# Kernel tuning notes

Measured on AMD Instinct MI355X. Metric: run time of the kernel, lower is better.

## Reference

```python
import jax, jax.numpy as jnp
import numpy as np

B, HI, WI, DIM = 4, 128, 128, 128
HO, WO = HI // 2, WI // 2
NUM_ITERS = 3
EPS_LN, EPS_A = 1e-5, 1e-6


def _nbr_idx(H, W):
    # NATTEN kernel_size=3 neighborhood with border clamping: window center is
    # clip(i, 1, H-2) so every position sees exactly 9 neighbors.
    r = 1
    ci = jnp.clip(jnp.arange(H), r, H - 1 - r)
    cj = jnp.clip(jnp.arange(W), r, W - 1 - r)
    off = jnp.arange(-1, 2)
    ri = ci[:, None] + off[None, :]  # (H,3)
    rj = cj[:, None] + off[None, :]  # (W,3)
    nbr = jnp.broadcast_to(ri[:, None, :, None], (H, W, 3, 3)).reshape(H, W, 9)
    nbc = jnp.broadcast_to(rj[None, :, None, :], (H, W, 3, 3)).reshape(H, W, 9)
    return nbr, nbc


def _ln(x, g, b):
    mu = jnp.mean(x, -1, keepdims=True)
    var = jnp.mean(jnp.square(x - mu), -1, keepdims=True)
    return (x - mu) * jax.lax.rsqrt(var + EPS_LN) * g + b


def setup_inputs() -> dict:
    key = jax.random.key(0)
    ks = jax.random.split(key, 10)
    s = DIM ** -0.5
    return {
        "x": jax.random.normal(ks[0], (B, HI * WI, DIM), jnp.float32),
        "conv_w": jax.random.normal(ks[1], (DIM, DIM, 3, 3), jnp.float32) * (2.0 / (DIM * 9)) ** 0.5,
        "q_w": jax.random.normal(ks[2], (DIM, DIM), jnp.float32) * s,
        "k_w": jax.random.normal(ks[3], (DIM, DIM), jnp.float32) * s,
        "v_w": jax.random.normal(ks[4], (DIM, DIM), jnp.float32) * s,
        "mlp_w1": jax.random.normal(ks[5], (DIM, 2 * DIM), jnp.float32) * s,
        "mlp_b1": jnp.zeros((2 * DIM,), jnp.float32),
        "mlp_w2": jax.random.normal(ks[6], (2 * DIM, DIM), jnp.float32) * (2 * DIM) ** -0.5,
        "mlp_b2": jnp.zeros((DIM,), jnp.float32),
        "ln_in_g": jnp.ones((DIM,), jnp.float32),
        "ln_in_b": jnp.zeros((DIM,), jnp.float32),
        "ln_out_g": jnp.ones((DIM,), jnp.float32),
        "ln_out_b": jnp.zeros((DIM,), jnp.float32),
        "tau": jnp.asarray(np.log(DIM ** -0.5), jnp.float32),
        "rpb": jax.random.normal(ks[7], (4, 9), jnp.float32) * 0.02,
    }


def reference(x, conv_w, q_w, k_w, v_w, mlp_w1, mlp_b1, mlp_w2, mlp_b2,
              ln_in_g, ln_in_b, ln_out_g, ln_out_b, tau, rpb):
    Bx = x.shape[0]
    nbr, nbc = _nbr_idx(HO, WO)
    q_idx = (nbr * WO + nbc).reshape(HO * WO, 9)  # flat seed index of each neighbor

    def to_groups(t):  # (B, Hi*Wi, D) -> (B, 4, Ho, Wo, D); 4 = 2x2 patch pixels (row-major)
        m = t.transpose(0, 2, 1).reshape(Bx, DIM, HO, 2, WO, 2)
        return m.transpose(0, 3, 5, 2, 4, 1).reshape(Bx, 4, HO, WO, DIM)

    k = to_groups(_ln(x, ln_in_g, ln_in_b) @ k_w)
    v = to_groups(x @ v_w)
    v_nb = v[:, :, nbr, nbc, :]  # (B,4,Ho,Wo,9,D) value neighborhoods (loop-invariant)

    x_map = x.transpose(0, 2, 1).reshape(Bx, DIM, HI, WI)
    seed = jax.lax.conv_general_dilated(x_map, conv_w, (2, 2), ((1, 1), (1, 1)),
                                        dimension_numbers=('NCHW', 'OIHW', 'NCHW'))
    x_out = _ln(seed.reshape(Bx, DIM, HO * WO).transpose(0, 2, 1), ln_out_g, ln_out_b)

    scale = jnp.exp(tau)
    flat_idx = jnp.broadcast_to(q_idx[None], (4, HO * WO, 9)).reshape(-1)
    attn = A_col = None
    for _ in range(NUM_ITERS):
        q = _ln(x_out, ln_out_g, ln_out_b) @ q_w
        q_nb = q.reshape(Bx, HO, WO, DIM)[:, nbr, nbc, :]  # (B,Ho,Wo,9,D)
        # na2d_qk(query=k, key=q): logits at key-grid position vs seed neighbors
        attn = jnp.einsum('bghwd,bhwtd->bghwt', k, q_nb)
        attn = jax.nn.softmax((attn + rpb.reshape(1, 4, 1, 1, 9)) * scale, axis=-1) + EPS_A
        # scatter-based column sums over seed tokens (doubly-stochastic step)
        attn_flat = attn.reshape(Bx, -1)
        col_sums = jax.vmap(
            lambda a: jax.ops.segment_sum(a, flat_idx, num_segments=HO * WO))(attn_flat)
        denom = col_sums[:, q_idx]  # (B, Ho*Wo, 9) gather back per-edge
        A_col = (attn.reshape(Bx, 4, HO * WO, 9) / (denom[:, None] + 1e-8)).reshape(Bx, 4, HO, WO, 9)
        # na2d_av(A_col, v) then sum over the 4 patch-pixel groups
        upd = jnp.einsum('bghwt,bghwtd->bhwd', A_col, v_nb).reshape(Bx, HO * WO, DIM)
        x_out = x_out + upd
        h = jax.nn.gelu(x_out @ mlp_w1 + mlp_b1, approximate=False) @ mlp_w2 + mlp_b2
        x_out = x_out + _ln(h, ln_out_g, ln_out_b)
    return x_out, attn, A_col
```

## Files before the change

kernel.cpp:

```cpp
#include <hip/hip_runtime.h>
#include <hip/hip_bf16.h>
#include <math.h>

#define BN 4
#define HIq 128
#define WIq 128
#define DIM 128
#define HOq 64
#define WOq 64
#define NPOS 4096
#define NTOK 16384
#define EPS_LN 1e-5f
#define EPS_A 1e-6f

typedef __attribute__((ext_vector_type(8))) short bf16x8;
typedef __attribute__((ext_vector_type(4))) float f32x4;

__device__ __forceinline__ unsigned short f2bf(float f) {
    unsigned int u = __float_as_uint(f);
    u = (u + 0x7FFFu + ((u >> 16) & 1u)) >> 16;
    return (unsigned short)u;
}

__device__ __forceinline__ int nb_index(int h, int w, int t) {
    int ch = min(max(h, 1), HOq - 2);
    int cw = min(max(w, 1), WOq - 2);
    int dr = t / 3 - 1, dc = t % 3 - 1;
    return (ch + dr) * WOq + (cw + dc);
}

__global__ void prep_ln_kernel(const float* __restrict__ x,
                               const float* __restrict__ g,
                               const float* __restrict__ bb,
                               unsigned short* __restrict__ x_bf,
                               unsigned short* __restrict__ xln_bf) {
    int tid = threadIdx.x, wv = tid >> 6, lane = tid & 63;
    long row = (long)blockIdx.x * 4 + wv;
    const float* xr = x + row * DIM;
    float v0 = xr[lane], v1 = xr[lane + 64];
    float s = v0 + v1, ss = v0 * v0 + v1 * v1;
    #pragma unroll
    for (int off = 32; off; off >>= 1) {
        s  += __shfl_xor(s, off, 64);
        ss += __shfl_xor(ss, off, 64);
    }
    float mu = s * (1.0f / DIM);
    float var = fmaxf(ss * (1.0f / DIM) - mu * mu, 0.0f);
    float rstd = rsqrtf(var + EPS_LN);
    x_bf[row * DIM + lane]        = f2bf(v0);
    x_bf[row * DIM + lane + 64]   = f2bf(v1);
    xln_bf[row * DIM + lane]      = f2bf((v0 - mu) * rstd * g[lane] + bb[lane]);
    xln_bf[row * DIM + lane + 64] = f2bf((v1 - mu) * rstd * g[lane + 64] + bb[lane + 64]);
}

__global__ void conv_wt_kernel(const float* __restrict__ cw, unsigned short* __restrict__ wt) {
    int o = blockIdx.x, tap = blockIdx.y, i = threadIdx.x;
    wt[(long)o * 1152 + tap * 128 + i] = f2bf(cw[((long)o * 128 + i) * 9 + tap]);
}

__global__ void wt_all_kernel(const float* __restrict__ kw, const float* __restrict__ vw,
                              const float* __restrict__ qw,
                              const float* __restrict__ w1, const float* __restrict__ w2,
                              unsigned short* __restrict__ kwt, unsigned short* __restrict__ vwt,
                              unsigned short* __restrict__ qwt,
                              unsigned short* __restrict__ w1t, unsigned short* __restrict__ w2t) {
    int o = blockIdx.x, i = threadIdx.x;
    kwt[o * DIM + i] = f2bf(kw[i * DIM + o]);
    vwt[o * DIM + i] = f2bf(vw[i * DIM + o]);
    qwt[o * DIM + i] = f2bf(qw[i * DIM + o]);
    w1t[(2 * o) * DIM + i]     = f2bf(w1[i * 256 + 2 * o]);
    w1t[(2 * o + 1) * DIM + i] = f2bf(w1[i * 256 + 2 * o + 1]);
    w2t[o * 256 + i]       = f2bf(w2[i * DIM + o]);
    w2t[o * 256 + 128 + i] = f2bf(w2[(128 + i) * DIM + o]);
}

__global__ __launch_bounds__(256) void conv_mfma_kernel(
        const unsigned short* __restrict__ x_bf,
        const unsigned short* __restrict__ wt,
        const float* __restrict__ ln_g, const float* __restrict__ ln_b,
        float* __restrict__ out_x) {
    __shared__ __align__(16) char smem[33792];
    unsigned short (*As)[40] = (unsigned short(*)[40])smem;
    unsigned short (*Bs)[40] = (unsigned short(*)[40])(smem + 5120);
    float (*o_s)[132]        = (float(*)[132])smem;

    int tid = threadIdx.x;
    int wv = tid >> 6, lane = tid & 63;
    int quad = lane >> 4, l15 = lane & 15;
    int wr = wv >> 1, wc = wv & 1;
    int b = blockIdx.x >> 6, ho = blockIdx.x & 63;

    f32x4 acc[2][4];
    #pragma unroll
    for (int mt = 0; mt < 2; ++mt)
        #pragma unroll
        for (int nt = 0; nt < 4; ++nt) acc[mt][nt] = (f32x4){0.f, 0.f, 0.f, 0.f};

    int m = tid >> 2, seg = tid & 3;
    for (int tap = 0; tap < 9; ++tap) {
        int kh = tap / 3, kw = tap % 3;
        int hi = 2 * ho - 1 + kh;
        int wi = 2 * m - 1 + kw;
        bool ok = (hi >= 0) && (hi < HIq) && (wi >= 0) && (wi < WIq);
        long arow = (((long)b * HIq + hi) * WIq + wi) * DIM;
        #pragma unroll
        for (int ib = 0; ib < 4; ++ib) {
            __syncthreads();
            int4 av = {0, 0, 0, 0};
            if (ok) av = *(const int4*)(x_bf + arow + ib * 32 + seg * 8);
            *(int4*)&As[m][seg * 8] = av;
            #pragma unroll
            for (int r2 = 0; r2 < 2; ++r2) {
                int lin = r2 * 256 + tid;
                int n = lin >> 2, sg = lin & 3;
                *(int4*)&Bs[n][sg * 8] =
                    *(const int4*)(wt + (long)n * 1152 + tap * 128 + ib * 32 + sg * 8);
            }
            __syncthreads();
            bf16x8 afr[2], bfr[4];
            #pragma unroll
            for (int mt = 0; mt < 2; ++mt)
                afr[mt] = *(bf16x8*)&As[wr * 32 + mt * 16 + l15][quad * 8];
            #pragma unroll
            for (int nt = 0; nt < 4; ++nt)
                bfr[nt] = *(bf16x8*)&Bs[wc * 64 + nt * 16 + l15][quad * 8];
            #pragma unroll
            for (int mt = 0; mt < 2; ++mt)
                #pragma unroll
                for (int nt = 0; nt < 4; ++nt)
                    acc[mt][nt] = __builtin_amdgcn_mfma_f32_16x16x32_bf16(
                        afr[mt], bfr[nt], acc[mt][nt], 0, 0, 0);
        }
    }
    __syncthreads();
    #pragma unroll
    for (int mt = 0; mt < 2; ++mt)
        #pragma unroll
        for (int r = 0; r < 4; ++r) {
            int wo = wr * 32 + mt * 16 + quad * 4 + r;
            #pragma unroll
            for (int nt = 0; nt < 4; ++nt) {
                int col = wc * 64 + nt * 16 + l15;
                o_s[wo][col] = acc[mt][nt][r];
            }
        }
    __syncthreads();

    {
        int r = tid >> 2, qq = tid & 3;
        float s = 0.f, ss = 0.f;
        #pragma unroll
        for (int j = 0; j < 32; ++j) {
            float v = o_s[r][qq * 32 + j];
            s += v; ss += v * v;
        }
        s  += __shfl_xor(s, 1, 64);  ss += __shfl_xor(ss, 1, 64);
        s  += __shfl_xor(s, 2, 64);  ss += __shfl_xor(ss, 2, 64);
        float mu = s * (1.0f / DIM);
        float var = fmaxf(ss * (1.0f / DIM) - mu * mu, 0.0f);
        float rstd = rsqrtf(var + EPS_LN);
        long outb = ((long)b * NPOS + ho * WOq) * DIM;
        float* xr = out_x + outb + (long)r * DIM + qq * 32;
        #pragma unroll
        for (int j = 0; j < 32; ++j) {
            int c = qq * 32 + j;
            xr[j] = (o_s[r][c] - mu) * rstd * ln_g[c] + ln_b[c];
        }
    }
}

__global__ __launch_bounds__(256) void kv_mfma_kernel(
        const unsigned short* __restrict__ x_bf,
        const unsigned short* __restrict__ xln_bf,
        const unsigned short* __restrict__ kwt,
        const unsigned short* __restrict__ vwt,
        unsigned short* __restrict__ k_bf, float* __restrict__ v_g) {
    __shared__ unsigned short Ak[64][40], Av[64][40];
    __shared__ unsigned short Bk[128][40], Bv[128][40];
    int tid = threadIdx.x;
    int wv = tid >> 6, lane = tid & 63;
    int quad = lane >> 4, l15 = lane & 15;
    int wr = wv >> 1, wc = wv & 1;
    long tokBase = (long)blockIdx.x * 64;

    f32x4 acck[2][4], accv[2][4];
    #pragma unroll
    for (int mt = 0; mt < 2; ++mt)
        #pragma unroll
        for (int nt = 0; nt < 4; ++nt) {
            acck[mt][nt] = (f32x4){0.f, 0.f, 0.f, 0.f};
            accv[mt][nt] = (f32x4){0.f, 0.f, 0.f, 0.f};
        }

    int m = tid >> 2, seg = tid & 3;
    #pragma unroll
    for (int ib = 0; ib < 4; ++ib) {
        __syncthreads();
        *(int4*)&Ak[m][seg * 8] = *(const int4*)(xln_bf + (tokBase + m) * DIM + ib * 32 + seg * 8);
        *(int4*)&Av[m][seg * 8] = *(const int4*)(x_bf   + (tokBase + m) * DIM + ib * 32 + seg * 8);
        #pragma unroll
        for (int r2 = 0; r2 < 2; ++r2) {
            int lin = r2 * 256 + tid;
            int n = lin >> 2, sg = lin & 3;
            *(int4*)&Bk[n][sg * 8] = *(const int4*)(kwt + (long)n * DIM + ib * 32 + sg * 8);
            *(int4*)&Bv[n][sg * 8] = *(const int4*)(vwt + (long)n * DIM + ib * 32 + sg * 8);
        }
        __syncthreads();
        bf16x8 ak[2], av2[2], bk[4], bv[4];
        #pragma unroll
        for (int mt = 0; mt < 2; ++mt) {
            ak[mt]  = *(bf16x8*)&Ak[wr * 32 + mt * 16 + l15][quad * 8];
            av2[mt] = *(bf16x8*)&Av[wr * 32 + mt * 16 + l15][quad * 8];
        }
        #pragma unroll
        for (int nt = 0; nt < 4; ++nt) {
            bk[nt] = *(bf16x8*)&Bk[wc * 64 + nt * 16 + l15][quad * 8];
            bv[nt] = *(bf16x8*)&Bv[wc * 64 + nt * 16 + l15][quad * 8];
        }
        #pragma unroll
        for (int mt = 0; mt < 2; ++mt)
            #pragma unroll
            for (int nt = 0; nt < 4; ++nt) {
                acck[mt][nt] = __builtin_amdgcn_mfma_f32_16x16x32_bf16(ak[mt],  bk[nt], acck[mt][nt], 0, 0, 0);
                accv[mt][nt] = __builtin_amdgcn_mfma_f32_16x16x32_bf16(av2[mt], bv[nt], accv[mt][nt], 0, 0, 0);
            }
    }
    #pragma unroll
    for (int mt = 0; mt < 2; ++mt)
        #pragma unroll
        for (int r = 0; r < 4; ++r) {
            long tok = tokBase + wr * 32 + mt * 16 + quad * 4 + r;
            int b = (int)(tok >> 14);
            int pix = (int)(tok & 16383);
            int ih = pix >> 7, iw = pix & 127;
            int g = (ih & 1) * 2 + (iw & 1);
            int pos = (ih >> 1) * WOq + (iw >> 1);
            long base = ((long)(b * 4 + g) * NPOS + pos) * DIM;
            #pragma unroll
            for (int nt = 0; nt < 4; ++nt) {
                int col = wc * 64 + nt * 16 + l15;
                k_bf[base + col] = f2bf(acck[mt][nt][r]);
                v_g[base + col]  = accv[mt][nt][r];
            }
        }
}

__global__ __launch_bounds__(256) void q_mfma_kernel(
        const float* __restrict__ x_out,
        const unsigned short* __restrict__ qwt,
        const float* __restrict__ ln_g, const float* __restrict__ ln_b,
        unsigned short* __restrict__ q) {
    __shared__ unsigned short sxbf[64][136];
    int tid = threadIdx.x;
    long base = (long)blockIdx.x * 64;

    {
        int r = tid >> 2, qq = tid & 3;
        const float* xr = x_out + (base + r) * DIM + qq * 32;
        float vv[32];
        float s = 0.f, ss = 0.f;
        #pragma unroll
        for (int j = 0; j < 8; ++j) {
            float4 v4 = *(const float4*)(xr + j * 4);
            vv[j * 4 + 0] = v4.x; vv[j * 4 + 1] = v4.y;
            vv[j * 4 + 2] = v4.z; vv[j * 4 + 3] = v4.w;
            s += v4.x + v4.y + v4.z + v4.w;
            ss += v4.x * v4.x + v4.y * v4.y + v4.z * v4.z + v4.w * v4.w;
        }
        s  += __shfl_xor(s, 1, 64);  ss += __shfl_xor(ss, 1, 64);
        s  += __shfl_xor(s, 2, 64);  ss += __shfl_xor(ss, 2, 64);
        float mu = s * (1.0f / DIM);
        float var = fmaxf(ss * (1.0f / DIM) - mu * mu, 0.0f);
        float rstd = rsqrtf(var + EPS_LN);
        #pragma unroll
        for (int j = 0; j < 32; ++j) {
            int c = qq * 32 + j;
            sxbf[r][c] = f2bf((vv[j] - mu) * rstd * ln_g[c] + ln_b[c]);
        }
    }
    __syncthreads();

    int wv = tid >> 6, lane = tid & 63;
    int quad = lane >> 4, l15 = lane & 15;
    f32x4 acc[4][2];
    #pragma unroll
    for (int mt = 0; mt < 4; ++mt)
        #pragma unroll
        for (int nt = 0; nt < 2; ++nt) acc[mt][nt] = (f32x4){0.f, 0.f, 0.f, 0.f};

    #pragma unroll
    for (int kb = 0; kb < 4; ++kb) {
        bf16x8 afr[4], bfr[2];
        #pragma unroll
        for (int mt = 0; mt < 4; ++mt)
            afr[mt] = *(bf16x8*)&sxbf[mt * 16 + l15][kb * 32 + quad * 8];
        #pragma unroll
        for (int nt = 0; nt < 2; ++nt) {
            int n = wv * 32 + nt * 16 + l15;
            bfr[nt] = *(const bf16x8*)(qwt + (long)n * DIM + kb * 32 + quad * 8);
        }
        #pragma unroll
        for (int mt = 0; mt < 4; ++mt)
            #pragma unroll
            for (int nt = 0; nt < 2; ++nt)
                acc[mt][nt] = __builtin_amdgcn_mfma_f32_16x16x32_bf16(
                    afr[mt], bfr[nt], acc[mt][nt], 0, 0, 0);
    }
    #pragma unroll
    for (int mt = 0; mt < 4; ++mt)
        #pragma unroll
        for (int r = 0; r < 4; ++r) {
            long tok = base + mt * 16 + quad * 4 + r;
            #pragma unroll
            for (int nt = 0; nt < 2; ++nt) {
                int col = wv * 32 + nt * 16 + l15;
                q[tok * DIM + col] = f2bf(acc[mt][nt][r]);
            }
        }
}

__global__ void zero_kernel(float* __restrict__ p, int n) {
    int i = blockIdx.x * blockDim.x + threadIdx.x;
    if (i < n) p[i] = 0.0f;
}

__global__ __launch_bounds__(256) void attn_mfma_kernel(
        const unsigned short* __restrict__ k_bf,
        const unsigned short* __restrict__ q_bf,
        const float* __restrict__ rpb,
        const float* __restrict__ tau,
        float* __restrict__ attn_out,
        float* __restrict__ col_sums) {
    __shared__ __align__(16) char smem[69632];
    unsigned short (*Ks)[136] = (unsigned short(*)[136])smem;
    unsigned short (*Qs)[136] = (unsigned short(*)[136])(smem + 17408);
    float (*S)[193]           = (float(*)[193])smem;

    int tid = threadIdx.x;
    int bid = blockIdx.x;
    int h = bid & 63, g = (bid >> 6) & 3, b = bid >> 8;
    int r0 = min(max(h, 1), HOq - 2) - 1;

    long kbase = ((long)(b * 4 + g) * NPOS + h * 64) * DIM;
    long qbase = ((long)b * NPOS + r0 * 64) * DIM;

    #pragma unroll
    for (int it = 0; it < 4; ++it) {
        int lin = it * 256 + tid;
        int row = lin >> 4, sg = lin & 15;
        *(int4*)&Ks[row][sg * 8] = *(const int4*)(k_bf + kbase + (long)row * DIM + sg * 8);
    }
    #pragma unroll
    for (int it = 0; it < 12; ++it) {
        int lin = it * 256 + tid;
        int row = lin >> 4, sg = lin & 15;
        *(int4*)&Qs[row][sg * 8] = *(const int4*)(q_bf + qbase + (long)row * DIM + sg * 8);
    }
    __syncthreads();

    int wv = tid >> 6, lane = tid & 63;
    int quad = lane >> 4, l15 = lane & 15;
    f32x4 acc[4][3];
    #pragma unroll
    for (int mt = 0; mt < 4; ++mt)
        #pragma unroll
        for (int nt = 0; nt < 3; ++nt) acc[mt][nt] = (f32x4){0.f, 0.f, 0.f, 0.f};

    #pragma unroll
    for (int kb = 0; kb < 4; ++kb) {
        bf16x8 afr[4], bfr[3];
        #pragma unroll
        for (int mt = 0; mt < 4; ++mt)
            afr[mt] = *(bf16x8*)&Ks[mt * 16 + l15][kb * 32 + quad * 8];
        #pragma unroll
        for (int nt = 0; nt < 3; ++nt)
            bfr[nt] = *(bf16x8*)&Qs[wv * 48 + nt * 16 + l15][kb * 32 + quad * 8];
        #pragma unroll
        for (int mt = 0; mt < 4; ++mt)
            #pragma unroll
            for (int nt = 0; nt < 3; ++nt)
                acc[mt][nt] = __builtin_amdgcn_mfma_f32_16x16x32_bf16(
                    afr[mt], bfr[nt], acc[mt][nt], 0, 0, 0);
    }
    __syncthreads();
    #pragma unroll
    for (int mt = 0; mt < 4; ++mt)
        #pragma unroll
        for (int nt = 0; nt < 3; ++nt)
            #pragma unroll
            for (int r = 0; r < 4; ++r)
                S[mt * 16 + quad * 4 + r][wv * 48 + nt * 16 + l15] = acc[mt][nt][r];
    __syncthreads();

    if (tid < 64) {
        int w = tid;
        int cw = min(max(w, 1), WOq - 2);
        float scale = expf(tau[0]);
        float l[9];
        #pragma unroll
        for (int t = 0; t < 9; ++t) {
            int j = (t / 3) * 64 + cw - 1 + (t % 3);
            l[t] = (S[w][j] + rpb[g * 9 + t]) * scale;
        }
        float m = l[0];
        #pragma unroll
        for (int t = 1; t < 9; ++t) m = fmaxf(m, l[t]);
        float e[9], s = 0.f;
        #pragma unroll
        for (int t = 0; t < 9; ++t) { e[t] = __expf(l[t] - m); s += e[t]; }
        float inv = 1.0f / s;
        long cell = (long)(b * 4 + g) * NPOS + h * 64 + w;
        #pragma unroll
        for (int t = 0; t < 9; ++t) {
            float a = e[t] * inv + EPS_A;
            int j = (t / 3) * 64 + cw - 1 + (t % 3);
            attn_out[cell * 9 + t] = a;
            atomicAdd(&col_sums[b * NPOS + r0 * 64 + j], a);
        }
    }
}

__global__ void acol_upd_kernel(const float* __restrict__ attn_out,
                                const float* __restrict__ col_sums,
                                const float* __restrict__ v_g,
                                float* __restrict__ acol_out,
                                float* __restrict__ x_out) {
    __shared__ float sA[36];
    int tid = threadIdx.x;
    int row = blockIdx.x;
    int b = row >> 12, pos = row & 4095;
    int h = pos >> 6, w = pos & 63;

    if (tid < 36) {
        int g = tid / 9, t = tid % 9;
        long ci = ((long)(b * 4 + g) * NPOS + pos) * 9 + t;
        float a = attn_out[ci];
        float cs = col_sums[b * NPOS + nb_index(h, w, t)];
        float A = a / (cs + 1e-8f);
        sA[tid] = A;
        acol_out[ci] = A;
    }
    __syncthreads();

    int nn[9];
    #pragma unroll
    for (int t = 0; t < 9; ++t) nn[t] = nb_index(h, w, t);

    float acc = 0.f;
    #pragma unroll
    for (int g = 0; g < 4; ++g) {
        const float* vb = v_g + (long)(b * 4 + g) * NPOS * DIM;
        #pragma unroll
        for (int t = 0; t < 9; ++t) {
            acc += sA[g * 9 + t] * vb[(long)nn[t] * DIM + tid];
        }
    }
    x_out[(long)row * DIM + tid] += acc;
}

__global__ __launch_bounds__(256) void mlp_mfma_kernel(
        float* __restrict__ x_out,
        const unsigned short* __restrict__ w1t,
        const unsigned short* __restrict__ w2t,
        const float* __restrict__ b1, const float* __restrict__ b2,
        const float* __restrict__ ln_g, const float* __restrict__ ln_b) {
    __shared__ __align__(16) char smem[51200];
    unsigned short (*sxbf)[136] = (unsigned short(*)[136])smem;
    unsigned short (*h_s)[264]  = (unsigned short(*)[264])(smem + 17408);
    float (*o_s)[132]           = (float(*)[132])smem;

    int tid = threadIdx.x;
    long base = (long)blockIdx.x * 64;
    int wv = tid >> 6, lane = tid & 63;
    int quad = lane >> 4, l15 = lane & 15;

    {
        int r = tid >> 2, seg = tid & 3;
        const float* xr = x_out + (base + r) * DIM + seg * 32;
        #pragma unroll
        for (int j = 0; j < 4; ++j) {
            float4 a = *(const float4*)(xr + j * 8);
            float4 c = *(const float4*)(xr + j * 8 + 4);
            unsigned short u[8] = {f2bf(a.x), f2bf(a.y), f2bf(a.z), f2bf(a.w),
                                   f2bf(c.x), f2bf(c.y), f2bf(c.z), f2bf(c.w)};
            *(int4*)&sxbf[r][seg * 32 + j * 8] = *(int4*)u;
        }
    }
    __syncthreads();

    f32x4 acc1[4][4];
    #pragma unroll
    for (int mt = 0; mt < 4; ++mt)
        #pragma unroll
        for (int nt = 0; nt < 4; ++nt) acc1[mt][nt] = (f32x4){0.f, 0.f, 0.f, 0.f};
    #pragma unroll
    for (int kb = 0; kb < 4; ++kb) {
        bf16x8 afr[4], bfr[4];
        #pragma unroll
        for (int mt = 0; mt < 4; ++mt)
            afr[mt] = *(bf16x8*)&sxbf[mt * 16 + l15][kb * 32 + quad * 8];
        #pragma unroll
        for (int nt = 0; nt < 4; ++nt) {
            int n = wv * 64 + nt * 16 + l15;
            bfr[nt] = *(const bf16x8*)(w1t + (long)n * DIM + kb * 32 + quad * 8);
        }
        #pragma unroll
        for (int mt = 0; mt < 4; ++mt)
            #pragma unroll
            for (int nt = 0; nt < 4; ++nt)
                acc1[mt][nt] = __builtin_amdgcn_mfma_f32_16x16x32_bf16(
                    afr[mt], bfr[nt], acc1[mt][nt], 0, 0, 0);
    }
    #pragma unroll
    for (int nt = 0; nt < 4; ++nt) {
        int col = wv * 64 + nt * 16 + l15;
        float bj = b1[col];
        #pragma unroll
        for (int mt = 0; mt < 4; ++mt)
            #pragma unroll
            for (int r = 0; r < 4; ++r) {
                int row = mt * 16 + quad * 4 + r;
                float hv = acc1[mt][nt][r] + bj;
                hv = 0.5f * hv * (1.0f + erff(hv * 0.70710678118654752f));
                h_s[row][col] = f2bf(hv);
            }
    }
    __syncthreads();

    f32x4 acc2[4][2];
    #pragma unroll
    for (int mt = 0; mt < 4; ++mt)
        #pragma unroll
        for (int nt = 0; nt < 2; ++nt) acc2[mt][nt] = (f32x4){0.f, 0.f, 0.f, 0.f};
    #pragma unroll
    for (int kb = 0; kb < 8; ++kb) {
        bf16x8 afr[4], bfr[2];
        #pragma unroll
        for (int mt = 0; mt < 4; ++mt)
            afr[mt] = *(bf16x8*)&h_s[mt * 16 + l15][kb * 32 + quad * 8];
        #pragma unroll
        for (int nt = 0; nt < 2; ++nt) {
            int n = wv * 32 + nt * 16 + l15;
            bfr[nt] = *(const bf16x8*)(w2t + (long)n * 256 + kb * 32 + quad * 8);
        }
        #pragma unroll
        for (int mt = 0; mt < 4; ++mt)
            #pragma unroll
            for (int nt = 0; nt < 2; ++nt)
                acc2[mt][nt] = __builtin_amdgcn_mfma_f32_16x16x32_bf16(
                    afr[mt], bfr[nt], acc2[mt][nt], 0, 0, 0);
    }
    __syncthreads();

    #pragma unroll
    for (int nt = 0; nt < 2; ++nt) {
        int col = wv * 32 + nt * 16 + l15;
        float bj = b2[col];
        #pragma unroll
        for (int mt = 0; mt < 4; ++mt)
            #pragma unroll
            for (int r = 0; r < 4; ++r)
                o_s[mt * 16 + quad * 4 + r][col] = acc2[mt][nt][r] + bj;
    }
    __syncthreads();

    {
        int r = tid >> 2, qq = tid & 3;
        float s = 0.f, ss = 0.f;
        #pragma unroll
        for (int j = 0; j < 32; ++j) {
            float v = o_s[r][qq * 32 + j];
            s += v; ss += v * v;
        }
        s  += __shfl_xor(s, 1, 64);  ss += __shfl_xor(ss, 1, 64);
        s  += __shfl_xor(s, 2, 64);  ss += __shfl_xor(ss, 2, 64);
        float mu = s * (1.0f / DIM);
        float var = fmaxf(ss * (1.0f / DIM) - mu * mu, 0.0f);
        float rstd = rsqrtf(var + EPS_LN);
        float* xr = x_out + (base + r) * DIM + qq * 32;
        #pragma unroll
        for (int j = 0; j < 32; ++j) {
            int c = qq * 32 + j;
            xr[j] = xr[j] + (o_s[r][c] - mu) * rstd * ln_g[c] + ln_b[c];
        }
    }
}

extern "C" void kernel_launch(void* const* d_in, const int* in_sizes, int n_in,
                              void* d_out, int out_size, void* d_ws, size_t ws_size,
                              hipStream_t stream) {
    const float* x        = (const float*)d_in[0];
    const float* conv_w   = (const float*)d_in[1];
    const float* q_w      = (const float*)d_in[2];
    const float* k_w      = (const float*)d_in[3];
    const float* v_w      = (const float*)d_in[4];
    const float* mlp_w1   = (const float*)d_in[5];
    const float* mlp_b1   = (const float*)d_in[6];
    const float* mlp_w2   = (const float*)d_in[7];
    const float* mlp_b2   = (const float*)d_in[8];
    const float* ln_in_g  = (const float*)d_in[9];
    const float* ln_in_b  = (const float*)d_in[10];
    const float* ln_out_g = (const float*)d_in[11];
    const float* ln_out_b = (const float*)d_in[12];
    const float* tau      = (const float*)d_in[13];
    const float* rpb      = (const float*)d_in[14];

    float* out_x    = (float*)d_out;
    float* out_attn = out_x + (long)BN * NPOS * DIM;
    float* out_acol = out_attn + (long)BN * 4 * NPOS * 9;

    char* ws = (char*)d_ws;
    unsigned short* k_bf = (unsigned short*)ws; ws += (long)BN * 4 * NPOS * DIM * 4;
    float* v_g = (float*)ws;            ws += (long)BN * 4 * NPOS * DIM * 4;
    unsigned short* x_bf = (unsigned short*)ws;
    unsigned short* q_bf = (unsigned short*)ws;
    ws += (long)BN * NTOK * DIM * 2;
    unsigned short* xln_bf = (unsigned short*)ws; ws += (long)BN * NTOK * DIM * 2;
    unsigned short* wt_conv = (unsigned short*)ws; ws += 1152L * DIM * 2;
    unsigned short* kwt = (unsigned short*)ws;     ws += (long)DIM * DIM * 2;
    unsigned short* vwt = (unsigned short*)ws;     ws += (long)DIM * DIM * 2;
    unsigned short* qwt = (unsigned short*)ws;     ws += (long)DIM * DIM * 2;
    unsigned short* w1t = (unsigned short*)ws;     ws += 256L * DIM * 2;
    unsigned short* w2t = (unsigned short*)ws;     ws += 256L * DIM * 2;
    float* col_sums = (float*)ws;       ws += (long)BN * NPOS * 4;

    prep_ln_kernel<<<16384, 256, 0, stream>>>(x, ln_in_g, ln_in_b, x_bf, xln_bf);
    conv_wt_kernel<<<dim3(128, 9), 128, 0, stream>>>(conv_w, wt_conv);
    wt_all_kernel<<<128, 128, 0, stream>>>(k_w, v_w, q_w, mlp_w1, mlp_w2,
                                           kwt, vwt, qwt, w1t, w2t);

    kv_mfma_kernel<<<1024, 256, 0, stream>>>(x_bf, xln_bf, kwt, vwt, k_bf, v_g);
    conv_mfma_kernel<<<256, 256, 0, stream>>>(x_bf, wt_conv, ln_out_g, ln_out_b, out_x);

    for (int it = 0; it < 3; ++it) {
        q_mfma_kernel<<<256, 256, 0, stream>>>(out_x, qwt, ln_out_g, ln_out_b, q_bf);
        zero_kernel<<<(BN * NPOS + 255) / 256, 256, 0, stream>>>(col_sums, BN * NPOS);
        attn_mfma_kernel<<<1024, 256, 0, stream>>>(k_bf, q_bf, rpb, tau, out_attn, col_sums);
        acol_upd_kernel<<<16384, 128, 0, stream>>>(out_attn, col_sums, v_g, out_acol, out_x);
        mlp_mfma_kernel<<<256, 256, 0, stream>>>(out_x, w1t, w2t, mlp_b1, mlp_b2,
                                                 ln_out_g, ln_out_b);
    }
}
```

Before: 344.5 us.

## Store V in bf16, pre-reduce column sums in LDS, load full-K conv tiles

V is stored as bf16 instead of fp32, halving the bytes the acol/update kernel gathers on each of the three iterations. The attention kernel accumulates column sums in a shared-memory array and issues one global atomic per column per block instead of one per edge. The conv kernel loads a whole 128-wide K slice per tap with one barrier pair instead of four, at the cost of more LDS. The bf16 V adds rounding error to the attention update.

```diff
diff --git a/kernel.cpp b/kernel.cpp
--- a/kernel.cpp
+++ b/kernel.cpp
@@ -20,6 +20,10 @@
     unsigned int u = __float_as_uint(f);
     u = (u + 0x7FFFu + ((u >> 16) & 1u)) >> 16;
     return (unsigned short)u;
+}
+
+__device__ __forceinline__ float bf2f(unsigned short u) {
+    return __uint_as_float((unsigned int)u << 16);
 }
 
 __device__ __forceinline__ int nb_index(int h, int w, int t) {
@@ -79,10 +83,10 @@
         const unsigned short* __restrict__ wt,
         const float* __restrict__ ln_g, const float* __restrict__ ln_b,
         float* __restrict__ out_x) {
-    __shared__ __align__(16) char smem[33792];
-    unsigned short (*As)[40] = (unsigned short(*)[40])smem;
-    unsigned short (*Bs)[40] = (unsigned short(*)[40])(smem + 5120);
-    float (*o_s)[132]        = (float(*)[132])smem;
+    __shared__ __align__(16) char smem[52224];
+    unsigned short (*As)[136] = (unsigned short(*)[136])smem;
+    unsigned short (*Bs)[136] = (unsigned short(*)[136])(smem + 17408);
+    float (*o_s)[132]         = (float(*)[132])smem;
 
     int tid = threadIdx.x;
     int wv = tid >> 6, lane = tid & 63;
@@ -96,34 +100,38 @@
         #pragma unroll
         for (int nt = 0; nt < 4; ++nt) acc[mt][nt] = (f32x4){0.f, 0.f, 0.f, 0.f};
 
-    int m = tid >> 2, seg = tid & 3;
     for (int tap = 0; tap < 9; ++tap) {
         int kh = tap / 3, kw = tap % 3;
         int hi = 2 * ho - 1 + kh;
-        int wi = 2 * m - 1 + kw;
-        bool ok = (hi >= 0) && (hi < HIq) && (wi >= 0) && (wi < WIq);
-        long arow = (((long)b * HIq + hi) * WIq + wi) * DIM;
+        bool hok = (hi >= 0) && (hi < HIq);
+        __syncthreads();
+        #pragma unroll
+        for (int it = 0; it < 4; ++it) {
+            int c = it * 256 + tid;
+            int row = c >> 4, sg = c & 15;
+            int wi = 2 * row - 1 + kw;
+            int4 av = {0, 0, 0, 0};
+            if (hok && wi >= 0 && wi < WIq)
+                av = *(const int4*)(x_bf + (((long)b * HIq + hi) * WIq + wi) * DIM + sg * 8);
+            *(int4*)&As[row][sg * 8] = av;
+        }
+        #pragma unroll
+        for (int it = 0; it < 8; ++it) {
+            int c = it * 256 + tid;
+            int row = c >> 4, sg = c & 15;
+            *(int4*)&Bs[row][sg * 8] =
+                *(const int4*)(wt + (long)row * 1152 + tap * 128 + sg * 8);
+        }
+        __syncthreads();
         #pragma unroll
         for (int ib = 0; ib < 4; ++ib) {
-            __syncthreads();
-            int4 av = {0, 0, 0, 0};
-            if (ok) av = *(const int4*)(x_bf + arow + ib * 32 + seg * 8);
-            *(int4*)&As[m][seg * 8] = av;
-            #pragma unroll
-            for (int r2 = 0; r2 < 2; ++r2) {
-                int lin = r2 * 256 + tid;
-                int n = lin >> 2, sg = lin & 3;
-                *(int4*)&Bs[n][sg * 8] =
-                    *(const int4*)(wt + (long)n * 1152 + tap * 128 + ib * 32 + sg * 8);
-            }
-            __syncthreads();
             bf16x8 afr[2], bfr[4];
             #pragma unroll
             for (int mt = 0; mt < 2; ++mt)
-                afr[mt] = *(bf16x8*)&As[wr * 32 + mt * 16 + l15][quad * 8];
+                afr[mt] = *(bf16x8*)&As[wr * 32 + mt * 16 + l15][ib * 32 + quad * 8];
             #pragma unroll
             for (int nt = 0; nt < 4; ++nt)
-                bfr[nt] = *(bf16x8*)&Bs[wc * 64 + nt * 16 + l15][quad * 8];
+                bfr[nt] = *(bf16x8*)&Bs[wc * 64 + nt * 16 + l15][ib * 32 + quad * 8];
             #pragma unroll
             for (int mt = 0; mt < 2; ++mt)
                 #pragma unroll
@@ -174,7 +182,7 @@
         const unsigned short* __restrict__ xln_bf,
         const unsigned short* __restrict__ kwt,
         const unsigned short* __restrict__ vwt,
-        unsigned short* __restrict__ k_bf, float* __restrict__ v_g) {
+        unsigned short* __restrict__ k_bf, unsigned short* __restrict__ v_bf) {
     __shared__ unsigned short Ak[64][40], Av[64][40];
     __shared__ unsigned short Bk[128][40], Bv[128][40];
     int tid = threadIdx.x;
@@ -240,7 +248,7 @@
             for (int nt = 0; nt < 4; ++nt) {
                 int col = wc * 64 + nt * 16 + l15;
                 k_bf[base + col] = f2bf(acck[mt][nt][r]);
-                v_g[base + col]  = accv[mt][nt][r];
+                v_bf[base + col] = f2bf(accv[mt][nt][r]);
             }
         }
 }
@@ -332,6 +340,7 @@
         float* __restrict__ attn_out,
         float* __restrict__ col_sums) {
     __shared__ __align__(16) char smem[69632];
+    __shared__ float colacc[192];
     unsigned short (*Ks)[136] = (unsigned short(*)[136])smem;
     unsigned short (*Qs)[136] = (unsigned short(*)[136])(smem + 17408);
     float (*S)[193]           = (float(*)[193])smem;
@@ -343,6 +352,8 @@
 
     long kbase = ((long)(b * 4 + g) * NPOS + h * 64) * DIM;
     long qbase = ((long)b * NPOS + r0 * 64) * DIM;
+
+    if (tid < 192) colacc[tid] = 0.f;
 
     #pragma unroll
     for (int it = 0; it < 4; ++it) {
@@ -415,14 +426,16 @@
             float a = e[t] * inv + EPS_A;
             int j = (t / 3) * 64 + cw - 1 + (t % 3);
             attn_out[cell * 9 + t] = a;
-            atomicAdd(&col_sums[b * NPOS + r0 * 64 + j], a);
-        }
-    }
+            atomicAdd(&colacc[j], a);
+        }
+    }
+    __syncthreads();
+    if (tid < 192) atomicAdd(&col_sums[b * NPOS + r0 * 64 + tid], colacc[tid]);
 }
 
 __global__ void acol_upd_kernel(const float* __restrict__ attn_out,
                                 const float* __restrict__ col_sums,
-                                const float* __restrict__ v_g,
+                                const unsigned short* __restrict__ v_bf,
                                 float* __restrict__ acol_out,
                                 float* __restrict__ x_out) {
     __shared__ float sA[36];
@@ -449,10 +462,10 @@
     float acc = 0.f;
     #pragma unroll
     for (int g = 0; g < 4; ++g) {
-        const float* vb = v_g + (long)(b * 4 + g) * NPOS * DIM;
+        const unsigned short* vb = v_bf + (long)(b * 4 + g) * NPOS * DIM;
         #pragma unroll
         for (int t = 0; t < 9; ++t) {
-            acc += sA[g * 9 + t] * vb[(long)nn[t] * DIM + tid];
+            acc += sA[g * 9 + t] * bf2f(vb[(long)nn[t] * DIM + tid]);
         }
     }
     x_out[(long)row * DIM + tid] += acc;
@@ -611,7 +624,7 @@
 
     char* ws = (char*)d_ws;
     unsigned short* k_bf = (unsigned short*)ws; ws += (long)BN * 4 * NPOS * DIM * 4;
-    float* v_g = (float*)ws;            ws += (long)BN * 4 * NPOS * DIM * 4;
+    unsigned short* v_bf = (unsigned short*)ws; ws += (long)BN * 4 * NPOS * DIM * 4;
     unsigned short* x_bf = (unsigned short*)ws;
     unsigned short* q_bf = (unsigned short*)ws;
     ws += (long)BN * NTOK * DIM * 2;
@@ -629,14 +642,14 @@
     wt_all_kernel<<<128, 128, 0, stream>>>(k_w, v_w, q_w, mlp_w1, mlp_w2,
                                            kwt, vwt, qwt, w1t, w2t);
 
-    kv_mfma_kernel<<<1024, 256, 0, stream>>>(x_bf, xln_bf, kwt, vwt, k_bf, v_g);
+    kv_mfma_kernel<<<1024, 256, 0, stream>>>(x_bf, xln_bf, kwt, vwt, k_bf, v_bf);
     conv_mfma_kernel<<<256, 256, 0, stream>>>(x_bf, wt_conv, ln_out_g, ln_out_b, out_x);
 
     for (int it = 0; it < 3; ++it) {
         q_mfma_kernel<<<256, 256, 0, stream>>>(out_x, qwt, ln_out_g, ln_out_b, q_bf);
         zero_kernel<<<(BN * NPOS + 255) / 256, 256, 0, stream>>>(col_sums, BN * NPOS);
         attn_mfma_kernel<<<1024, 256, 0, stream>>>(k_bf, q_bf, rpb, tau, out_attn, col_sums);
-        acol_upd_kernel<<<16384, 128, 0, stream>>>(out_attn, col_sums, v_g, out_acol, out_x);
+        acol_upd_kernel<<<16384, 128, 0, stream>>>(out_attn, col_sums, v_bf, out_acol, out_x);
         mlp_mfma_kernel<<<256, 256, 0, stream>>>(out_x, w1t, w2t, mlp_b1, mlp_b2,
                                                  ln_out_g, ln_out_b);
     }
```

Result: faster. 324.7 us (-5.8%).
